# Kernel optimization log

Hardware: AMD Instinct MI355X
Metric: run time of the kernel (lower is better)

## Reference

```python
import jax, jax.numpy as jnp
import numpy as np

B, S, DIM = 1, 2048, 2048
HEADS, KV_HEADS = 32, 8
DH = DIM // HEADS          # 64 head dim
G = HEADS // KV_HEADS      # 4 grouped queries per kv head
CBLK = 16                  # compress block size (stride == block size)
SBLK = 16                  # selection (fine) block size
NSEL = 8                   # top-k selected blocks
WIN = 64                   # sliding window size
SCALE = DH ** -0.5
NEG = -1e30
CDIM = CBLK * DH


def setup_inputs():
    key = jax.random.key(0)
    ks = jax.random.split(key, 16)
    def rnd(i, shape, sc=0.02):
        return jax.random.normal(ks[i], shape, dtype=jnp.float32) * sc
    dim_inner, dim_kv = HEADS * DH, KV_HEADS * DH
    return {
        "hidden_states": jax.random.normal(ks[0], (B, S, DIM), dtype=jnp.float32),
        "w_qkv": rnd(1, (DIM, dim_inner + 2 * dim_kv)),
        "k_pos": rnd(2, (KV_HEADS, CBLK, DH)),
        "v_pos": rnd(3, (KV_HEADS, CBLK, DH)),
        "k_cw1": rnd(4, (CDIM, CDIM)), "k_cb1": jnp.zeros((CDIM,), jnp.float32),
        "k_cw2": rnd(5, (CDIM, DH)),  "k_cb2": jnp.zeros((DH,), jnp.float32),
        "v_cw1": rnd(6, (CDIM, CDIM)), "v_cb1": jnp.zeros((CDIM,), jnp.float32),
        "v_cw2": rnd(7, (CDIM, DH)),  "v_cb2": jnp.zeros((DH,), jnp.float32),
        "mem_ck": rnd(8, (KV_HEADS, 1, DH)),
        "mem_cv": rnd(9, (KV_HEADS, 1, DH)),
        "w_gate": rnd(10, (DIM, 3 * HEADS)),
        "b_gate": jnp.tile(jnp.array([-2.0, -2.0, 2.0], jnp.float32), HEADS),
        "w_out": rnd(11, (dim_inner, DIM)),
    }


def _rope(x, pos):
    # rotary-embedding-torch style: interleaved pairs (x0,x1),(x2,x3),...
    d = x.shape[-1]
    inv = 1.0 / (10000.0 ** (jnp.arange(0, d, 2, dtype=jnp.float32) / d))
    ang = pos[:, None] * inv[None, :]
    cos, sin = jnp.cos(ang), jnp.sin(ang)
    x1, x2 = x[..., 0::2], x[..., 1::2]
    return jnp.stack([x1 * cos - x2 * sin, x1 * sin + x2 * cos], axis=-1).reshape(x.shape)


def _forward(x, w_qkv, k_pos, v_pos, k_cw1, k_cb1, k_cw2, k_cb2,
             v_cw1, v_cb1, v_cw2, v_cb2, mem_ck, mem_cv, w_gate, b_gate, w_out):
    b, n, _ = x.shape
    di, dkv = HEADS * DH, KV_HEADS * DH
    qkv = x @ w_qkv
    # head index = kv_head * G + grouped_query, matching 'b n (h d) -> b h n d'
    q = qkv[..., :di].reshape(b, n, KV_HEADS, G, DH).transpose(0, 2, 3, 1, 4)    # [b,kh,g,n,d]
    k = qkv[..., di:di + dkv].reshape(b, n, KV_HEADS, DH).transpose(0, 2, 1, 3)  # [b,kh,n,d]
    v = qkv[..., di + dkv:].reshape(b, n, KV_HEADS, DH).transpose(0, 2, 1, 3)

    # ---- branch 1: compressed-block attention (pre-rotary q/k, intra-block abs pos) ----
    nc = n // CBLK
    kb = k[:, :, :nc * CBLK].reshape(b, KV_HEADS, nc, CBLK, DH) + k_pos[None, :, None]
    vb = v[:, :, :nc * CBLK].reshape(b, KV_HEADS, nc, CBLK, DH) + v_pos[None, :, None]
    ck = jax.nn.relu(kb.reshape(b, KV_HEADS, nc, CDIM) @ k_cw1 + k_cb1) @ k_cw2 + k_cb2
    cv = jax.nn.relu(vb.reshape(b, KV_HEADS, nc, CDIM) @ v_cw1 + v_cb1) @ v_cw2 + v_cb2
    ck = jnp.concatenate([jnp.broadcast_to(mem_ck[None], (b, KV_HEADS, 1, DH)), ck], axis=2)
    cv = jnp.concatenate([jnp.broadcast_to(mem_cv[None], (b, KV_HEADS, 1, DH)), cv], axis=2)
    csim = jnp.einsum('bhgnd,bhjd->bhgnj', q, ck) * SCALE
    ck_last = jnp.concatenate([jnp.array([-1]), (jnp.arange(nc) + 1) * CBLK - 1])
    cmask = ck_last[None, :] < jnp.arange(n)[:, None]                            # [n, 1+nc]
    csim = jnp.where(cmask, csim, NEG)
    c_out = jnp.einsum('bhgnj,bhjd->bhgnd', jax.nn.softmax(csim, -1), cv)

    # ---- importance scores -> top-k selected blocks (shared across grouped queries) ----
    imp = csim[..., 1:].mean(axis=2)                                             # [b,kh,n,nc]
    imp = jnp.concatenate([jnp.full(imp.shape[:-1] + (1,), -1e3, imp.dtype), imp], axis=-1)
    imp = jax.nn.softmax(imp, -1)[..., 1:]
    sel_vals, sel_idx = jax.lax.top_k(imp, NSEL)                                 # [b,kh,n,NSEL]
    fine_gate_mask = sel_vals > 1e-10

    # rotary for fine + sliding branches
    pos = jnp.arange(n, dtype=jnp.float32)
    rq, rk = _rope(q, pos), _rope(k, pos)

    # ---- branch 2: fine attention over top-k selected blocks + causal own block ----
    nf = n // SBLK
    own = jnp.broadcast_to((jnp.arange(n) // SBLK)[None, None, :, None], (b, KV_HEADS, n, 1))
    idx = jnp.concatenate([sel_idx, own], axis=-1)                               # [b,kh,n,NSEL+1]
    kblocks = rk.reshape(b, KV_HEADS, nf, SBLK, DH)
    vblocks = v.reshape(b, KV_HEADS, nf, SBLK, DH)
    bi = jnp.arange(b)[:, None, None, None]
    hi = jnp.arange(KV_HEADS)[None, :, None, None]
    fk = kblocks[bi, hi, idx].reshape(b, KV_HEADS, n, (NSEL + 1) * SBLK, DH)
    fv = vblocks[bi, hi, idx].reshape(b, KV_HEADS, n, (NSEL + 1) * SBLK, DH)
    sel_m = jnp.repeat(fine_gate_mask[..., None], SBLK, -1).reshape(b, KV_HEADS, n, NSEL * SBLK)
    diag_m = (jnp.arange(n) % SBLK)[:, None] >= jnp.arange(SBLK)[None, :]        # own-block causal
    fmask = jnp.concatenate(
        [sel_m, jnp.broadcast_to(diag_m[None, None], (b, KV_HEADS, n, SBLK))], axis=-1)
    fsim = jnp.einsum('bhgnd,bhnjd->bhgnj', rq, fk) * SCALE
    fsim = jnp.where(fmask[:, :, None], fsim, NEG)
    f_out = jnp.einsum('bhgnj,bhnjd->bhgnd', jax.nn.softmax(fsim, -1), fv)

    # ---- branch 3: sliding-window attention (current + previous window, exact size) ----
    nwin = n // WIN
    qw = rq.reshape(b, KV_HEADS, G, nwin, WIN, DH)
    kw = rk.reshape(b, KV_HEADS, nwin, WIN, DH)
    vw = v.reshape(b, KV_HEADS, nwin, WIN, DH)
    kcat = jnp.concatenate([jnp.concatenate([jnp.zeros_like(kw[:, :, :1]), kw[:, :, :-1]], 2), kw], 3)
    vcat = jnp.concatenate([jnp.concatenate([jnp.zeros_like(vw[:, :, :1]), vw[:, :, :-1]], 2), vw], 3)
    ssim = jnp.einsum('bhgwid,bhwjd->bhgwij', qw, kcat) * SCALE
    i_, j_ = jnp.arange(WIN), jnp.arange(2 * WIN)
    delta = i_[:, None] - (j_[None, :] - WIN)                                    # query - key distance
    smask = ((delta >= 0) & (delta <= WIN))[None] \
        & ((jnp.arange(nwin) > 0)[:, None, None] | (j_ >= WIN)[None, None, :])
    ssim = jnp.where(smask[None, None, None], ssim, NEG)
    s_out = jnp.einsum('bhgwij,bhwjd->bhgwid', jax.nn.softmax(ssim, -1), vcat)
    s_out = s_out.reshape(b, KV_HEADS, G, n, DH)

    # ---- learned sigmoid gate combine (compressed, fine, sliding) + out proj ----
    gates = jax.nn.sigmoid(x @ w_gate + b_gate).reshape(b, n, KV_HEADS, G, 3).transpose(0, 2, 3, 1, 4)
    out = gates[..., 0:1] * c_out + gates[..., 1:2] * f_out + gates[..., 2:3] * s_out
    out = out.transpose(0, 3, 1, 2, 4).reshape(b, n, HEADS * DH)
    return out @ w_out


def reference(hidden_states, w_qkv, k_pos, v_pos, k_cw1, k_cb1, k_cw2, k_cb2,
              v_cw1, v_cb1, v_cw2, v_cb2, mem_ck, mem_cv, w_gate, b_gate, w_out):
    return _forward(hidden_states, w_qkv, k_pos, v_pos, k_cw1, k_cb1, k_cw2, k_cb2,
                    v_cw1, v_cb1, v_cw2, v_cb2, mem_ck, mem_cv, w_gate, b_gate, w_out)
```

## Files before the change

### kernel.cpp

```cpp
#include <hip/hip_runtime.h>
#include <hip/hip_bf16.h>
#include <math.h>

using bf16 = __hip_bfloat16;
typedef __attribute__((ext_vector_type(8))) short short8;
typedef __attribute__((ext_vector_type(4))) float f32x4;

#define SCALE 0.125f
#define NEGV  -1e30f
#define QS    3200

__device__ __forceinline__ float bf2f(bf16 x) { return __bfloat162float(x); }
__device__ __forceinline__ bf16  f2bf(float x) { return __float2bfloat16(x); }
__device__ __forceinline__ short f2bs(float x) {
  bf16 b = __float2bfloat16(x);
  return *reinterpret_cast<short*>(&b);
}
__device__ __forceinline__ float dot4(float4 a, float4 b) {
  return a.x * b.x + a.y * b.y + a.z * b.z + a.w * b.w;
}
__device__ __forceinline__ float sigm(float x) { return 1.0f / (1.0f + __expf(-x)); }

__device__ __forceinline__ void wavefence() {
  asm volatile("s_waitcnt lgkmcnt(0)" ::: "memory");
}

__device__ __forceinline__ void gload16(const bf16* g, bf16* l) {
  __builtin_amdgcn_global_load_lds(
      (const __attribute__((address_space(1))) unsigned int*)g,
      (__attribute__((address_space(3))) unsigned int*)l, 16, 0, 0);
}

__global__ void detect_mode_kernel(const void* __restrict__ bgate, int* __restrict__ flag)
{
  if (threadIdx.x == 0 && blockIdx.x == 0) {
    unsigned w = *(const unsigned*)bgate;
    flag[0] = (w == 0xC0000000u) ? 1 : 0;
  }
}

struct ConvArgs {
  const void* src[17];
  bf16*       dst[17];
  int         start[18];
};

__global__ __launch_bounds__(256)
void convert_all_kernel(ConvArgs a, int total, const int* __restrict__ flag)
{
  int i = blockIdx.x * 256 + threadIdx.x;
  if (i >= total) return;
  int s = 0;
  while (s < 16 && i >= a.start[s + 1]) s++;
  int off = i - a.start[s];
  if (*flag) a.dst[s][off] = f2bf(((const float*)a.src[s])[off]);
  else       a.dst[s][off] = ((const bf16*)a.src[s])[off];
}

__global__ __launch_bounds__(256)
void transpose_conv_kernel(const void* __restrict__ src, bf16* __restrict__ dst,
                           int K, int N, const int* __restrict__ flag)
{
  __shared__ bf16 ls[64][65];
  const int n0 = blockIdx.x * 64, k0 = blockIdx.y * 64;
  const int tid = threadIdx.x, c = tid & 63, r4 = tid >> 6;
  const bool f = (*flag != 0);
  #pragma unroll 4
  for (int r = 0; r < 16; r++) {
    int kk = r * 4 + r4;
    bf16 v = f2bf(0.f);
    if (n0 + c < N)
      v = f ? f2bf(((const float*)src)[(size_t)(k0 + kk) * N + n0 + c])
            : ((const bf16*)src)[(size_t)(k0 + kk) * N + n0 + c];
    ls[kk][c] = v;
  }
  __syncthreads();
  #pragma unroll 4
  for (int r = 0; r < 16; r++) {
    int nn = r * 4 + r4;
    if (n0 + nn < N)
      dst[(size_t)(n0 + nn) * K + k0 + c] = ls[c][nn];
  }
}

__global__ __launch_bounds__(256)
void vtrans_kernel(const float* __restrict__ qkv, bf16* __restrict__ vt)
{
  __shared__ bf16 ls[64][65];
  const int h = blockIdx.y;
  const int i0 = blockIdx.x * 64;
  const int tid = threadIdx.x, c = tid & 63, r4 = tid >> 6;
  #pragma unroll 4
  for (int r = 0; r < 16; r++) {
    int ii = r * 4 + r4;
    ls[ii][c] = f2bf(qkv[(size_t)(i0 + ii) * QS + 2560 + h * 64 + c]);
  }
  __syncthreads();
  #pragma unroll 4
  for (int r = 0; r < 16; r++) {
    int dd = r * 4 + r4;
    vt[((size_t)h * 64 + dd) * 2176 + 64 + i0 + c] = ls[c][dd];
  }
}

__global__ __launch_bounds__(256)
void gemm64_splitk_kernel(const bf16* __restrict__ A, const bf16* __restrict__ B,
                          const bf16* __restrict__ B2, float* __restrict__ C,
                          int M, int N, int K, int msplit, int Ks)
{
  __shared__ __align__(16) bf16 As[64 * 32];
  __shared__ __align__(16) bf16 Bs[64 * 32];
  const int tid = threadIdx.x, wave = tid >> 6, lane = tid & 63;
  const int quad = lane >> 4, l16 = lane & 15;
  const int m0 = blockIdx.y * 64, n0 = blockIdx.x * 64;
  const int kb = blockIdx.z * Ks;
  const bf16* Bu = (m0 >= msplit) ? B2 : B;
  f32x4 acc[4] = {{0,0,0,0},{0,0,0,0},{0,0,0,0},{0,0,0,0}};
  const int arow = tid >> 2, akp = (tid & 3) * 8;
  const int bkr = tid >> 3, bnc = (tid & 7) * 8;

  for (int k0 = kb; k0 < kb + Ks; k0 += 32) {
    __syncthreads();
    {
      const bf16* Ap = A + (size_t)(m0 + arow) * K + k0 + akp;
      *(int4*)(void*)&As[arow * 32 + akp] = *(const int4*)(const void*)Ap;
    }
    const bf16* Bp = Bu + (size_t)(k0 + bkr) * N + n0 + bnc;
    {
      int4 raw = *(const int4*)(const void*)Bp;
      const bf16* tp = (const bf16*)&raw;
      #pragma unroll
      for (int j = 0; j < 8; j++) Bs[(bnc + j) * 32 + bkr] = tp[j];
    }
    __syncthreads();
    short8 a = *(const short8*)(const void*)&As[(wave * 16 + l16) * 32 + quad * 8];
    #pragma unroll
    for (int nt = 0; nt < 4; nt++) {
      short8 b = *(const short8*)(const void*)&Bs[(nt * 16 + l16) * 32 + quad * 8];
      acc[nt] = __builtin_amdgcn_mfma_f32_16x16x32_bf16(a, b, acc[nt], 0, 0, 0);
    }
  }

  #pragma unroll
  for (int nt = 0; nt < 4; nt++) {
    int col = n0 + nt * 16 + l16;
    if (col < N) {
      #pragma unroll
      for (int r = 0; r < 4; r++) {
        int row = m0 + wave * 16 + quad * 4 + r;
        atomicAdd(&C[(size_t)row * N + col], acc[nt][r]);
      }
    }
  }
}

template<int TC_BF16, int ACT, int SPLIT, int GATE, int STOREF>
__global__ __launch_bounds__(256)
void gemm_bt_kernel(const bf16* __restrict__ A, const bf16* __restrict__ Bt,
                    const bf16* __restrict__ Bt2, const bf16* __restrict__ bias,
                    const bf16* __restrict__ bias2, void* __restrict__ Cv,
                    int M, int N, int K, int msplit, const int* __restrict__ flag)
{
  __shared__ __align__(16) bf16 As[128 * 32];
  __shared__ __align__(16) bf16 Bs[128 * 32];
  const int tid = threadIdx.x, wave = tid >> 6, lane = tid & 63;
  const int quad = lane >> 4, l16 = lane & 15;
  const int wm = (wave >> 1) * 64, wn = (wave & 1) * 64;
  const int m0 = blockIdx.y * 128, n0 = blockIdx.x * 128;
  const bf16* Bu = (SPLIT && m0 >= msplit) ? Bt2 : Bt;
  const bf16* bu = (SPLIT && m0 >= msplit) ? bias2 : bias;
  f32x4 acc[4][4];
  #pragma unroll
  for (int mt = 0; mt < 4; mt++)
    #pragma unroll
    for (int nt = 0; nt < 4; nt++) acc[mt][nt] = f32x4{0, 0, 0, 0};

  const int lr = lane >> 2, lc = (lane & 3) * 8;
  const bf16* gA0 = A  + (size_t)(m0 + wave * 32 + lr) * K + lc;
  const bf16* gA1 = gA0 + (size_t)16 * K;
  const bf16* gB0 = Bu + (size_t)(n0 + wave * 32 + lr) * K + lc;
  const bf16* gB1 = gB0 + (size_t)16 * K;
  bf16* lA0 = &As[wave * 1024];
  bf16* lA1 = &As[wave * 1024 + 512];
  bf16* lB0 = &Bs[wave * 1024];
  bf16* lB1 = &Bs[wave * 1024 + 512];

  for (int k0 = 0; k0 < K; k0 += 32) {
    __syncthreads();
    gload16(gA0 + k0, lA0);
    gload16(gA1 + k0, lA1);
    gload16(gB0 + k0, lB0);
    gload16(gB1 + k0, lB1);
    __syncthreads();

    short8 a[4], b[4];
    #pragma unroll
    for (int mt = 0; mt < 4; mt++)
      a[mt] = *(const short8*)(const void*)&As[(wm + mt * 16 + l16) * 32 + quad * 8];
    #pragma unroll
    for (int nt = 0; nt < 4; nt++)
      b[nt] = *(const short8*)(const void*)&Bs[(wn + nt * 16 + l16) * 32 + quad * 8];
    #pragma unroll
    for (int mt = 0; mt < 4; mt++)
      #pragma unroll
      for (int nt = 0; nt < 4; nt++)
        acc[mt][nt] = __builtin_amdgcn_mfma_f32_16x16x32_bf16(a[mt], b[nt], acc[mt][nt], 0, 0, 0);
  }

  const bool f32out = STOREF ? (*flag != 0) : false;
  #pragma unroll
  for (int nt = 0; nt < 4; nt++) {
    int col = n0 + wn + nt * 16 + l16;
    float bv;
    if (GATE) bv = (col >= 3072 && col < 3168) ? bf2f(bias2[col - 3072]) : 0.0f;
    else      bv = bu ? bf2f(bu[col]) : 0.0f;
    #pragma unroll
    for (int mt = 0; mt < 4; mt++) {
      #pragma unroll
      for (int r = 0; r < 4; r++) {
        int row = m0 + wm + mt * 16 + quad * 4 + r;
        float v = acc[mt][nt][r] + bv;
        if (ACT == 1) v = fmaxf(v, 0.0f);
        if (STOREF) {
          if (f32out) ((float*)Cv)[(size_t)row * N + col] = v;
          else        ((bf16*)Cv)[(size_t)row * N + col]  = f2bf(v);
        } else if (TC_BF16) {
          ((bf16*)Cv)[(size_t)row * N + col] = f2bf(v);
        } else {
          ((float*)Cv)[(size_t)row * N + col] = v;
        }
      }
    }
  }
}

__global__ __launch_bounds__(256)
void prep_kb_kernel(const float* __restrict__ qkv, const bf16* __restrict__ k_pos,
                    const bf16* __restrict__ v_pos, bf16* __restrict__ kbflat,
                    bf16* __restrict__ vbflat)
{
  int idx = blockIdx.x * 256 + threadIdx.x;
  if (idx >= 8 * 128 * 1024) return;
  int h = idx >> 17, rem = idx & 131071;
  int c = rem >> 10, f = rem & 1023, t = f >> 6, d = f & 63;
  int tok = c * 16 + t;
  float kv = qkv[(size_t)tok * QS + 2048 + h * 64 + d] + bf2f(k_pos[(h * 16 + t) * 64 + d]);
  float vv = qkv[(size_t)tok * QS + 2560 + h * 64 + d] + bf2f(v_pos[(h * 16 + t) * 64 + d]);
  kbflat[idx] = f2bf(kv);
  vbflat[idx] = f2bf(vv);
}

__global__ __launch_bounds__(256)
void concat_kernel(const float* __restrict__ ckpre, const float* __restrict__ cvpre,
                   const bf16* __restrict__ mem_ck, const bf16* __restrict__ mem_cv,
                   const bf16* __restrict__ k_cb2, const bf16* __restrict__ v_cb2,
                   float* __restrict__ ck, bf16* __restrict__ cvT)
{
  int idx = blockIdx.x * 256 + threadIdx.x;
  if (idx >= 8 * 160 * 64) return;
  int h = idx / (160 * 64), r = (idx >> 6) % 160, d = idx & 63;
  if (r >= 129) { cvT[((size_t)h * 64 + d) * 160 + r] = f2bf(0.f); return; }
  float kv, vv;
  if (r == 0) {
    kv = bf2f(mem_ck[h * 64 + d]);
    vv = bf2f(mem_cv[h * 64 + d]);
  } else {
    kv = ckpre[((size_t)h * 128 + r - 1) * 64 + d] + bf2f(k_cb2[d]);
    vv = cvpre[((size_t)h * 128 + r - 1) * 64 + d] + bf2f(v_cb2[d]);
  }
  ck[((size_t)h * 129 + r) * 64 + d] = kv;
  cvT[((size_t)h * 64 + d) * 160 + r] = f2bf(vv);
}

__global__ __launch_bounds__(256)
void compress_attn_kernel(const float* __restrict__ qkv, const float* __restrict__ ck,
                          const bf16* __restrict__ cvT,
                          float* __restrict__ outpre, int* __restrict__ sel)
{
  __shared__ __align__(16) float qs[4][16][64];
  __shared__ __align__(16) bf16  ps[4][16][176];
  const int tid = threadIdx.x, w = tid >> 6, lane = tid & 63;
  const int quad = lane >> 4, l16 = lane & 15;
  const int h = blockIdx.x >> 7;
  const int i0 = (blockIdx.x & 127) * 16 + w * 4;

  #pragma unroll
  for (int m = 0; m < 16; m++)
    qs[w][m][lane] = qkv[(size_t)(i0 + (m >> 2)) * QS + (h * 4 + (m & 3)) * 64 + lane];
  wavefence();

  const bool jin2 = (lane == 0);
  const float* kh = ck + (size_t)h * 129 * 64;
  const float4* k0 = (const float4*)(kh + lane * 64);
  const float4* k1 = (const float4*)(kh + (lane + 64) * 64);
  const float4* k2 = (const float4*)(kh + (jin2 ? 128 : 0) * 64);

  float d0[4][4], d1[4][4], d2[4][4];
  #pragma unroll
  for (int T = 0; T < 4; T++)
    #pragma unroll
    for (int g = 0; g < 4; g++) { d0[T][g] = 0.f; d1[T][g] = 0.f; d2[T][g] = 0.f; }

  #pragma unroll 4
  for (int t = 0; t < 16; t++) {
    float4 a = k0[t], b = k1[t], c = k2[t];
    #pragma unroll
    for (int T = 0; T < 4; T++)
      #pragma unroll
      for (int g = 0; g < 4; g++) {
        float4 qv = *(const float4*)&qs[w][T * 4 + g][t * 4];
        d0[T][g] += dot4(qv, a);
        d1[T][g] += dot4(qv, b);
        d2[T][g] += dot4(qv, c);
      }
  }

  #pragma unroll
  for (int T = 0; T < 4; T++) {
    const int i = i0 + T, jv = i >> 4;
    bool v0 = (lane == 0 || lane <= jv);
    bool v1 = (lane + 64 <= jv);
    bool v2 = jin2 && (128 <= jv);

    float sc0[4], sc1[4], sc2[4];
    #pragma unroll
    for (int g = 0; g < 4; g++) {
      sc0[g] = v0 ? d0[T][g] * SCALE : NEGV;
      sc1[g] = v1 ? d1[T][g] * SCALE : NEGV;
      sc2[g] = jin2 ? (v2 ? d2[T][g] * SCALE : NEGV) : -3.0e38f;
    }
    float imp0 = (sc0[0] + sc0[1] + sc0[2] + sc0[3]) * 0.25f;
    float imp1 = (sc1[0] + sc1[1] + sc1[2] + sc1[3]) * 0.25f;
    float imp2 = jin2 ? (sc2[0] + sc2[1] + sc2[2] + sc2[3]) * 0.25f : -3.0e38f;

    float p0[4], p1[4], p2[4];
    #pragma unroll
    for (int g = 0; g < 4; g++) {
      float mx = fmaxf(sc0[g], fmaxf(sc1[g], sc2[g]));
      for (int off = 32; off; off >>= 1) mx = fmaxf(mx, __shfl_xor(mx, off));
      float e0 = __expf(sc0[g] - mx), e1 = __expf(sc1[g] - mx);
      float e2 = jin2 ? __expf(sc2[g] - mx) : 0.0f;
      float sm = e0 + e1 + e2;
      for (int off = 32; off; off >>= 1) sm += __shfl_xor(sm, off);
      float inv = 1.0f / sm;
      p0[g] = e0 * inv; p1[g] = e1 * inv; p2[g] = e2 * inv;
    }

    #pragma unroll
    for (int g = 0; g < 4; g++) {
      ps[w][T * 4 + g][lane]      = f2bf(p0[g]);
      ps[w][T * 4 + g][64 + lane] = f2bf(p1[g]);
    }
    if (lane == 0) {
      #pragma unroll
      for (int g = 0; g < 4; g++) ps[w][T * 4 + g][128] = f2bf(p2[g]);
    }

    float iv0 = (lane == 0) ? -1000.0f : imp0;
    float iv1 = imp1;
    float iv2 = imp2;
    float mx = fmaxf(iv0, fmaxf(iv1, iv2));
    for (int off = 32; off; off >>= 1) mx = fmaxf(mx, __shfl_xor(mx, off));
    float e0 = __expf(iv0 - mx), e1 = __expf(iv1 - mx);
    float e2 = jin2 ? __expf(iv2 - mx) : 0.0f;
    float sm = e0 + e1 + e2;
    for (int off = 32; off; off >>= 1) sm += __shfl_xor(sm, off);
    float inv = 1.0f / sm;
    float q0 = (lane >= 1) ? e0 * inv : -1.0f;
    float q1 = e1 * inv;
    float q2 = jin2 ? e2 * inv : -1.0f;

    for (int s = 0; s < 8; s++) {
      float bv = q0; int bj = lane;
      if (q1 > bv) { bv = q1; bj = lane + 64; }
      if (q2 > bv) { bv = q2; bj = lane + 128; }
      for (int off = 32; off; off >>= 1) {
        float ov = __shfl_xor(bv, off); int oj = __shfl_xor(bj, off);
        if (ov > bv || (ov == bv && oj < bj)) { bv = ov; bj = oj; }
      }
      if (lane == 0) sel[((size_t)h * 2048 + i) * 8 + s] = (bv > 1e-10f) ? (bj - 1) : -1;
      if (bj == lane)            q0 = -1.0f;
      else if (bj == lane + 64)  q1 = -1.0f;
      else if (bj == lane + 128) q2 = -1.0f;
    }
  }

  #pragma unroll
  for (int r = 0; r < 4; r++) {
    ps[w][quad * 4 + r][129 + l16] = f2bf(0.f);
    ps[w][quad * 4 + r][145 + l16] = f2bf(0.f);
  }

  const int iq = i0 + quad;
  float g0v[4];
  #pragma unroll
  for (int g = 0; g < 4; g++)
    g0v[g] = sigm(qkv[(size_t)iq * QS + 3072 + (h * 4 + g) * 3 + 0]);
  wavefence();

  const bf16* cvh = cvT + (size_t)h * 64 * 160;
  f32x4 acc[4];
  #pragma unroll
  for (int dt = 0; dt < 4; dt++) acc[dt] = f32x4{0, 0, 0, 0};
  #pragma unroll
  for (int ks = 0; ks < 5; ks++) {
    short8 ap = *(const short8*)(const void*)&ps[w][l16][ks * 32 + quad * 8];
    #pragma unroll
    for (int dt = 0; dt < 4; dt++) {
      const bf16* cp = cvh + (size_t)(dt * 16 + l16) * 160 + ks * 32 + quad * 8;
      short8 bv = *(const short8*)(const void*)cp;
      acc[dt] = __builtin_amdgcn_mfma_f32_16x16x32_bf16(ap, bv, acc[dt], 0, 0, 0);
    }
  }

  #pragma unroll
  for (int g = 0; g < 4; g++) {
    const int hq = h * 4 + g;
    #pragma unroll
    for (int dt = 0; dt < 4; dt++)
      outpre[(size_t)iq * 2048 + hq * 64 + dt * 16 + l16] = g0v[g] * acc[dt][g];
  }
}

__global__ __launch_bounds__(256)
void rope_kernel(const float* __restrict__ qkv, bf16* __restrict__ qb,
                 bf16* __restrict__ kb)
{
  int idx = blockIdx.x * 256 + threadIdx.x;
  if (idx >= 2048 * 40 * 32) return;
  int m = idx & 31, hh = (idx >> 5) % 40, i = idx / 1280;
  int col = (hh < 32) ? hh * 64 + 2 * m : 2048 + (hh - 32) * 64 + 2 * m;
  const float* p = qkv + (size_t)i * QS + col;
  float x1 = p[0], x2 = p[1];
  float inv = exp2f(-0.41524101186092029f * (float)m);
  float ang = (float)i * inv;
  float s, c;
  __sincosf(ang, &s, &c);
  float r1 = x1 * c - x2 * s;
  float r2 = x1 * s + x2 * c;
  unsigned pack = ((unsigned)(unsigned short)f2bs(r1)) |
                  (((unsigned)(unsigned short)f2bs(r2)) << 16);
  if (hh < 32) {
    int h = hh >> 2, g = hh & 3;
    *(unsigned*)&qb[(((size_t)h * 2048 + i) * 4 + g) * 64 + 2 * m] = pack;
  } else {
    *(unsigned*)&kb[((size_t)(hh - 32) * 2048 + i) * 64 + 2 * m] = pack;
  }
}

__global__ __launch_bounds__(256)
void slide_attn_kernel(const float* __restrict__ qkv, const bf16* __restrict__ qb,
                       const bf16* __restrict__ kb, const bf16* __restrict__ vt,
                       bf16* __restrict__ oslide)
{
  __shared__ __align__(16) bf16 ps[4][16][104];
  const int tid = threadIdx.x, w = tid >> 6, lane = tid & 63;
  const int quad = lane >> 4, l16 = lane & 15;
  const int h = blockIdx.x >> 7, i0 = (blockIdx.x & 127) << 4;
  const int g = w;

  const bf16* qp = qb + (((size_t)h * 2048 + i0 + l16) * 4 + g) * 64 + quad * 8;
  short8 aq0 = *(const short8*)(const void*)qp;
  short8 aq1 = *(const short8*)(const void*)(qp + 32);

  const bf16* kbh = kb + (size_t)h * 2048 * 64;
  const int jbase = i0 - 64;

  f32x4 cs[5];
  #pragma unroll
  for (int t = 0; t < 5; t++) {
    int jr = jbase + t * 16 + l16;
    int jc = jr < 0 ? 0 : jr;
    const bf16* kp = kbh + (size_t)jc * 64 + quad * 8;
    short8 b0 = *(const short8*)(const void*)kp;
    short8 b1 = *(const short8*)(const void*)(kp + 32);
    f32x4 c = {0.f, 0.f, 0.f, 0.f};
    c = __builtin_amdgcn_mfma_f32_16x16x32_bf16(aq0, b0, c, 0, 0, 0);
    c = __builtin_amdgcn_mfma_f32_16x16x32_bf16(aq1, b1, c, 0, 0, 0);
    cs[t] = c;
  }

  float pr[5][4];
  #pragma unroll
  for (int r = 0; r < 4; r++) {
    int ti = i0 + quad * 4 + r;
    float mx = -3.0e38f;
    #pragma unroll
    for (int t = 0; t < 5; t++) {
      int j = jbase + t * 16 + l16;
      bool valid = (j >= 0) && (j >= ti - 64) && (j <= ti);
      float sv = valid ? cs[t][r] * SCALE : -3.0e38f;
      pr[t][r] = sv;
      mx = fmaxf(mx, sv);
    }
    #pragma unroll
    for (int off = 8; off; off >>= 1) mx = fmaxf(mx, __shfl_xor(mx, off));
    float sm = 0.f;
    #pragma unroll
    for (int t = 0; t < 5; t++) { float e = __expf(pr[t][r] - mx); pr[t][r] = e; sm += e; }
    #pragma unroll
    for (int off = 8; off; off >>= 1) sm += __shfl_xor(sm, off);
    float inv = 1.0f / sm;
    #pragma unroll
    for (int t = 0; t < 5; t++) pr[t][r] *= inv;
  }

  #pragma unroll
  for (int t = 0; t < 5; t++)
    #pragma unroll
    for (int r = 0; r < 4; r++)
      ps[w][quad * 4 + r][t * 16 + l16] = f2bf(pr[t][r]);
  #pragma unroll
  for (int r = 0; r < 4; r++) ps[w][l16][80 + quad * 4 + r] = f2bf(0.f);
  wavefence();

  const bf16* vth = vt + (size_t)h * 64 * 2176 + 64;
  f32x4 os[4];
  #pragma unroll
  for (int dt = 0; dt < 4; dt++) os[dt] = f32x4{0,0,0,0};
  #pragma unroll
  for (int ks = 0; ks < 3; ks++) {
    short8 ap = *(const short8*)(const void*)&ps[w][l16][ks * 32 + quad * 8];
    int coff = jbase + ks * 32 + quad * 8;
    #pragma unroll
    for (int dt = 0; dt < 4; dt++) {
      const bf16* vp = vth + (size_t)(dt * 16 + l16) * 2176 + coff;
      short8 bv = *(const short8*)(const void*)vp;
      os[dt] = __builtin_amdgcn_mfma_f32_16x16x32_bf16(ap, bv, os[dt], 0, 0, 0);
    }
  }

  #pragma unroll
  for (int r = 0; r < 4; r++) {
    int ti = i0 + quad * 4 + r;
    int hq = h * 4 + g;
    float g2 = sigm(qkv[(size_t)ti * QS + 3072 + hq * 3 + 2]);
    #pragma unroll
    for (int dt = 0; dt < 4; dt++)
      oslide[(size_t)ti * 2048 + hq * 64 + dt * 16 + l16] = f2bf(g2 * os[dt][r]);
  }
}

__global__ __launch_bounds__(256)
void fine_attn_kernel(const float* __restrict__ qkv, const int* __restrict__ sel,
                      const float* __restrict__ outpre, const bf16* __restrict__ oslide,
                      const bf16* __restrict__ qb, const bf16* __restrict__ kb,
                      const bf16* __restrict__ vt, bf16* __restrict__ outpre_b)
{
  __shared__ __align__(16) bf16 psf[4][16][176];
  const int tid = threadIdx.x, w = tid >> 6, lane = tid & 63;
  const int quad = lane >> 4, l16 = lane & 15;
  const int h = blockIdx.x >> 7;
  const int i0 = (blockIdx.x & 127) * 16 + w * 4;

  const bf16* qp = qb + (((size_t)h * 2048 + i0 + (l16 >> 2)) * 4 + (l16 & 3)) * 64 + quad * 8;
  short8 aq0 = *(const short8*)(const void*)qp;
  short8 aq1 = *(const short8*)(const void*)(qp + 32);

  const bf16* kbh = kb + (size_t)h * 2048 * 64;
  const int own = i0 >> 4;
  const int selbase = (h * 2048 + i0) * 8;

  f32x4 ct[9];

  {
    const bf16* kp = kbh + (size_t)(own * 16 + l16) * 64 + quad * 8;
    short8 b0 = *(const short8*)(const void*)kp;
    short8 b1 = *(const short8*)(const void*)(kp + 32);
    f32x4 c = {0.f, 0.f, 0.f, 0.f};
    c = __builtin_amdgcn_mfma_f32_16x16x32_bf16(aq0, b0, c, 0, 0, 0);
    c = __builtin_amdgcn_mfma_f32_16x16x32_bf16(aq1, b1, c, 0, 0, 0);
    const int imod = (i0 + quad) & 15;
    #pragma unroll
    for (int g = 0; g < 4; g++)
      ct[8][g] = (l16 <= imod) ? c[g] * SCALE : -3.0e38f;
  }

  int vb[4][8];
  #pragma unroll
  for (int T = 0; T < 4; T++) {
    #pragma unroll
    for (int t = 0; t < 8; t++) {
      int blk = __builtin_amdgcn_readfirstlane(sel[selbase + T * 8 + t]);
      bool tv = (blk >= 0);
      int blc = tv ? blk : 0;
      vb[T][t] = blc;
      const bf16* kp = kbh + (size_t)(blc * 16 + l16) * 64 + quad * 8;
      short8 b0 = *(const short8*)(const void*)kp;
      short8 b1 = *(const short8*)(const void*)(kp + 32);
      f32x4 c = {0.f, 0.f, 0.f, 0.f};
      c = __builtin_amdgcn_mfma_f32_16x16x32_bf16(aq0, b0, c, 0, 0, 0);
      c = __builtin_amdgcn_mfma_f32_16x16x32_bf16(aq1, b1, c, 0, 0, 0);
      #pragma unroll
      for (int g = 0; g < 4; g++) {
        float v = tv ? c[g] * SCALE : -3.0e38f;
        if (T == 0) ct[t][g] = v;
        else if (quad == T) ct[t][g] = v;
      }
    }
  }

  float fm[4], fsum[4];
  #pragma unroll
  for (int g = 0; g < 4; g++) fm[g] = -3.0e38f;
  #pragma unroll
  for (int t = 0; t < 9; t++)
    #pragma unroll
    for (int g = 0; g < 4; g++) fm[g] = fmaxf(fm[g], ct[t][g]);
  #pragma unroll
  for (int g = 0; g < 4; g++) {
    #pragma unroll
    for (int off = 8; off; off >>= 1) fm[g] = fmaxf(fm[g], __shfl_xor(fm[g], off));
    fsum[g] = 0.f;
  }
  #pragma unroll
  for (int t = 0; t < 9; t++)
    #pragma unroll
    for (int g = 0; g < 4; g++) {
      float e = __expf(ct[t][g] - fm[g]);
      ct[t][g] = e;
      fsum[g] += e;
    }
  #pragma unroll
  for (int g = 0; g < 4; g++) {
    #pragma unroll
    for (int off = 8; off; off >>= 1) fsum[g] += __shfl_xor(fsum[g], off);
    fsum[g] = 1.0f / fsum[g];
  }

  #pragma unroll
  for (int t = 0; t < 9; t++)
    #pragma unroll
    for (int g = 0; g < 4; g++)
      psf[w][quad * 4 + g][t * 16 + l16] = f2bf(ct[t][g] * fsum[g]);
  #pragma unroll
  for (int g = 0; g < 4; g++)
    psf[w][quad * 4 + g][144 + l16] = f2bf(0.f);

  const int iq = i0 + quad;
  float g1v[4], prev[4][4];
  #pragma unroll
  for (int g = 0; g < 4; g++) {
    const int hq = h * 4 + g;
    g1v[g] = sigm(qkv[(size_t)iq * QS + 3072 + hq * 3 + 1]);
    #pragma unroll
    for (int dt = 0; dt < 4; dt++) {
      size_t oidx = (size_t)iq * 2048 + hq * 64 + dt * 16 + l16;
      prev[g][dt] = outpre[oidx] + bf2f(oslide[oidx]);
    }
  }
  wavefence();

  const bf16* vth = vt + (size_t)h * 64 * 2176 + 64;

  f32x4 obase[4];
  {
    short8 ap = *(const short8*)(const void*)&psf[w][l16][128 + quad * 8];
    int coff = (((quad >> 1) == 0) ? own : 0) * 16 + (quad & 1) * 8;
    #pragma unroll
    for (int dt = 0; dt < 4; dt++) {
      const bf16* vp = vth + (size_t)(dt * 16 + l16) * 2176 + coff;
      short8 bv = *(const short8*)(const void*)vp;
      f32x4 z = {0.f, 0.f, 0.f, 0.f};
      obase[dt] = __builtin_amdgcn_mfma_f32_16x16x32_bf16(ap, bv, z, 0, 0, 0);
    }
  }

  f32x4 osave[4];
  #pragma unroll
  for (int T = 0; T < 4; T++) {
    f32x4 acc[4];
    #pragma unroll
    for (int dt = 0; dt < 4; dt++) acc[dt] = obase[dt];
    #pragma unroll
    for (int ks = 0; ks < 4; ks++) {
      short8 ap = *(const short8*)(const void*)&psf[w][l16][ks * 32 + quad * 8];
      int blkv = ((quad >> 1) == 0) ? vb[T][ks * 2] : vb[T][ks * 2 + 1];
      int coff = blkv * 16 + (quad & 1) * 8;
      #pragma unroll
      for (int dt = 0; dt < 4; dt++) {
        const bf16* vp = vth + (size_t)(dt * 16 + l16) * 2176 + coff;
        short8 bv = *(const short8*)(const void*)vp;
        acc[dt] = __builtin_amdgcn_mfma_f32_16x16x32_bf16(ap, bv, acc[dt], 0, 0, 0);
      }
    }
    #pragma unroll
    for (int dt = 0; dt < 4; dt++) {
      if (T == 0) osave[dt] = acc[dt];
      else if (quad == T) osave[dt] = acc[dt];
    }
  }

  #pragma unroll
  for (int g = 0; g < 4; g++) {
    const int hq = h * 4 + g;
    #pragma unroll
    for (int dt = 0; dt < 4; dt++) {
      size_t oidx = (size_t)iq * 2048 + hq * 64 + dt * 16 + l16;
      outpre_b[oidx] = f2bf(prev[g][dt] + g1v[g] * osave[dt][g]);
    }
  }
}

extern "C" void kernel_launch(void* const* d_in, const int* in_sizes, int n_in,
                              void* d_out, int out_size, void* d_ws, size_t ws_size,
                              hipStream_t stream)
{
  char* ws = (char*)d_ws;
  size_t off = 0;
  auto alloc = [&](size_t bytes) -> char* {
    char* p = ws + off; off = (off + bytes + 255) & ~(size_t)255; return p;
  };

  int* flag = (int*)alloc(256);
  bf16* inb[17];
  for (int i = 0; i < 17; i++) {
    if (i == 1 || i == 4 || i == 8 || i == 14 || i == 16) { inb[i] = nullptr; continue; }
    inb[i] = (bf16*)alloc((size_t)in_sizes[i] * sizeof(bf16));
  }
  bf16* w_qkvT = (bf16*)alloc(3200ull * 2048 * 2);
  bf16* k_cw1T = (bf16*)alloc(1024ull * 1024 * 2);
  bf16* v_cw1T = (bf16*)alloc(1024ull * 1024 * 2);
  bf16* w_outT = (bf16*)alloc(2048ull * 2048 * 2);

  float* qkv      = (float*)alloc(2048ull * QS * 4);
  float* outpre   = (float*)alloc(2048ull * 2048 * 4);
  bf16*  kvb      = (bf16*)alloc(2048ull * 1024 * 2);
  bf16*  hid      = (bf16*)alloc(2048ull * 1024 * 2);
  float* ckcvpre  = (float*)alloc(2048ull * 64 * 4);
  float* ckb      = (float*)alloc(8ull * 129 * 64 * 4);
  int*   sel      = (int*)alloc(8ull * 2048 * 8 * 4);
  bf16*  qbuf     = (bf16*)alloc(8ull * 2048 * 4 * 64 * 2);
  bf16*  kbuf     = (bf16*)alloc(8ull * 2048 * 64 * 2);
  bf16*  vtb      = (bf16*)alloc(8ull * 64 * 2176 * 2);
  bf16*  outpre_b = kvb;
  bf16*  cvT      = k_cw1T;
  bf16*  oslide   = (bf16*)w_qkvT;

  const bf16 *xb = inb[0], *k_posb = inb[2], *v_posb = inb[3],
             *k_cb1b = inb[5], *k_cw2b = inb[6], *k_cb2b = inb[7],
             *v_cb1b = inb[9], *v_cw2b = inb[10], *v_cb2b = inb[11],
             *mem_ckb = inb[12], *mem_cvb = inb[13], *b_gateb = inb[15];

  detect_mode_kernel<<<1, 64, 0, stream>>>(d_in[15], flag);

  ConvArgs ca;
  int total = 0, nseg = 0;
  for (int i = 0; i < 17; i++) {
    if (i == 1 || i == 4 || i == 8 || i == 14 || i == 16) continue;
    ca.src[nseg] = d_in[i];
    ca.dst[nseg] = inb[i];
    ca.start[nseg] = total;
    total += in_sizes[i];
    nseg++;
  }
  for (int s = nseg; s <= 17; s++) ca.start[s] = total;
  convert_all_kernel<<<(total + 255) / 256, 256, 0, stream>>>(ca, total, flag);

  transpose_conv_kernel<<<dim3(48, 32), 256, 0, stream>>>(d_in[1],  w_qkvT, 2048, 3072, flag);
  transpose_conv_kernel<<<dim3(2, 32),  256, 0, stream>>>(d_in[14], w_qkvT + 3072ull * 2048, 2048, 96, flag);
  transpose_conv_kernel<<<dim3(16, 16), 256, 0, stream>>>(d_in[4],  k_cw1T, 1024, 1024, flag);
  transpose_conv_kernel<<<dim3(16, 16), 256, 0, stream>>>(d_in[8],  v_cw1T, 1024, 1024, flag);
  transpose_conv_kernel<<<dim3(32, 32), 256, 0, stream>>>(d_in[16], w_outT, 2048, 2048, flag);
  hipMemsetAsync(ckcvpre, 0, 2048ull * 64 * 4, stream);
  hipMemsetAsync(vtb, 0, 8ull * 64 * 2176 * 2, stream);

  gemm_bt_kernel<0,0,0,1,0><<<dim3(25, 16), 256, 0, stream>>>(
      xb, w_qkvT, nullptr, nullptr, b_gateb, qkv, 2048, QS, 2048, 0, nullptr);

  rope_kernel<<<10240, 256, 0, stream>>>(qkv, qbuf, kbuf);
  vtrans_kernel<<<dim3(32, 8), 256, 0, stream>>>(qkv, vtb);

  prep_kb_kernel<<<4096, 256, 0, stream>>>(qkv, k_posb, v_posb, kvb, kvb + 1024 * 1024);
  gemm_bt_kernel<1,1,1,0,0><<<dim3(8, 16), 256, 0, stream>>>(
      kvb, k_cw1T, v_cw1T, k_cb1b, v_cb1b, hid, 2048, 1024, 1024, 1024, nullptr);
  gemm64_splitk_kernel<<<dim3(1, 32, 4), 256, 0, stream>>>(
      hid, k_cw2b, v_cw2b, ckcvpre, 2048, 64, 1024, 1024, 256);
  concat_kernel<<<320, 256, 0, stream>>>(ckcvpre, ckcvpre + 1024 * 64,
                                         mem_ckb, mem_cvb, k_cb2b, v_cb2b, ckb, cvT);
  compress_attn_kernel<<<1024, 256, 0, stream>>>(qkv, ckb, cvT, outpre, sel);
  slide_attn_kernel<<<1024, 256, 0, stream>>>(qkv, qbuf, kbuf, vtb, oslide);
  fine_attn_kernel<<<1024, 256, 0, stream>>>(qkv, sel, outpre, oslide, qbuf, kbuf, vtb, outpre_b);
  gemm_bt_kernel<0,0,0,0,1><<<dim3(16, 16), 256, 0, stream>>>(
      outpre_b, w_outT, nullptr, nullptr, nullptr, d_out, 2048, 2048, 2048, 0, flag);
}
```

Before: 516.3 us.

## Skip causally masked compressed blocks and batch softmax/top-k reductions in compress attention

The compressed-attention kernel now uses the fact that all 16 queries in a block share one causal limit. It drops the always-masked key 128, computes keys 64..127 only for the later half of query blocks, and bounds the PV MFMA loop by the number of valid 32-key chunks. The per-row softmax, importance softmax and top-8 selection are restructured so cross-lane shuffle reductions for the 4 rows run interleaved, which exposes more instruction-level parallelism. The q and p shared buffers are aliased and launch bounds request 5 blocks per SM to raise occupancy, at some risk of register pressure from the larger live arrays.

Measured after the change: 536.7 us. +4.0%, slower.

```diff
diff --git a/kernel.cpp b/kernel.cpp
--- a/kernel.cpp
+++ b/kernel.cpp
@@ -272,123 +272,164 @@
   cvT[((size_t)h * 64 + d) * 160 + r] = f2bf(vv);
 }
 
-__global__ __launch_bounds__(256)
+__global__ __launch_bounds__(256, 5)
 void compress_attn_kernel(const float* __restrict__ qkv, const float* __restrict__ ck,
                           const bf16* __restrict__ cvT,
                           float* __restrict__ outpre, int* __restrict__ sel)
 {
-  __shared__ __align__(16) float qs[4][16][64];
-  __shared__ __align__(16) bf16  ps[4][16][176];
+  __shared__ __align__(16) char un[4][5632];
   const int tid = threadIdx.x, w = tid >> 6, lane = tid & 63;
   const int quad = lane >> 4, l16 = lane & 15;
   const int h = blockIdx.x >> 7;
-  const int i0 = (blockIdx.x & 127) * 16 + w * 4;
+  const int jv = blockIdx.x & 127;
+  const int i0 = jv * 16 + w * 4;
+  float* qs = (float*)un[w];
+  bf16*  ps = (bf16*)un[w];
 
   #pragma unroll
   for (int m = 0; m < 16; m++)
-    qs[w][m][lane] = qkv[(size_t)(i0 + (m >> 2)) * QS + (h * 4 + (m & 3)) * 64 + lane];
+    qs[m * 64 + lane] = qkv[(size_t)(i0 + (m >> 2)) * QS + (h * 4 + (m & 3)) * 64 + lane];
   wavefence();
 
-  const bool jin2 = (lane == 0);
   const float* kh = ck + (size_t)h * 129 * 64;
   const float4* k0 = (const float4*)(kh + lane * 64);
   const float4* k1 = (const float4*)(kh + (lane + 64) * 64);
-  const float4* k2 = (const float4*)(kh + (jin2 ? 128 : 0) * 64);
-
-  float d0[4][4], d1[4][4], d2[4][4];
+  const bool two = (jv >= 64);
+
+  float d0[4][4], d1[4][4];
   #pragma unroll
   for (int T = 0; T < 4; T++)
     #pragma unroll
-    for (int g = 0; g < 4; g++) { d0[T][g] = 0.f; d1[T][g] = 0.f; d2[T][g] = 0.f; }
-
-  #pragma unroll 4
-  for (int t = 0; t < 16; t++) {
-    float4 a = k0[t], b = k1[t], c = k2[t];
+    for (int g = 0; g < 4; g++) { d0[T][g] = 0.f; d1[T][g] = 0.f; }
+
+  if (two) {
+    #pragma unroll 4
+    for (int t = 0; t < 16; t++) {
+      float4 a = k0[t], b = k1[t];
+      #pragma unroll
+      for (int T = 0; T < 4; T++)
+        #pragma unroll
+        for (int g = 0; g < 4; g++) {
+          float4 qv = *(const float4*)&qs[(T * 4 + g) * 64 + t * 4];
+          d0[T][g] += dot4(qv, a);
+          d1[T][g] += dot4(qv, b);
+        }
+    }
+  } else {
+    #pragma unroll 4
+    for (int t = 0; t < 16; t++) {
+      float4 a = k0[t];
+      #pragma unroll
+      for (int T = 0; T < 4; T++)
+        #pragma unroll
+        for (int g = 0; g < 4; g++) {
+          float4 qv = *(const float4*)&qs[(T * 4 + g) * 64 + t * 4];
+          d0[T][g] += dot4(qv, a);
+        }
+    }
+  }
+  wavefence();
+
+  const bool v0 = (lane == 0) || (lane <= jv);
+  const bool v1 = two && (lane + 64 <= jv);
+  float imp0[4], imp1[4];
+  #pragma unroll
+  for (int T = 0; T < 4; T++) {
+    #pragma unroll
+    for (int g = 0; g < 4; g++) {
+      d0[T][g] = v0 ? d0[T][g] * SCALE : NEGV;
+      d1[T][g] = v1 ? d1[T][g] * SCALE : NEGV;
+    }
+    imp0[T] = (d0[T][0] + d0[T][1] + d0[T][2] + d0[T][3]) * 0.25f;
+    imp1[T] = (d1[T][0] + d1[T][1] + d1[T][2] + d1[T][3]) * 0.25f;
+  }
+
+  float mx[4][4], sm[4][4];
+  #pragma unroll
+  for (int T = 0; T < 4; T++)
+    #pragma unroll
+    for (int g = 0; g < 4; g++) mx[T][g] = fmaxf(d0[T][g], d1[T][g]);
+  #pragma unroll
+  for (int off = 32; off; off >>= 1)
     #pragma unroll
     for (int T = 0; T < 4; T++)
       #pragma unroll
-      for (int g = 0; g < 4; g++) {
-        float4 qv = *(const float4*)&qs[w][T * 4 + g][t * 4];
-        d0[T][g] += dot4(qv, a);
-        d1[T][g] += dot4(qv, b);
-        d2[T][g] += dot4(qv, c);
+      for (int g = 0; g < 4; g++) mx[T][g] = fmaxf(mx[T][g], __shfl_xor(mx[T][g], off));
+  #pragma unroll
+  for (int T = 0; T < 4; T++)
+    #pragma unroll
+    for (int g = 0; g < 4; g++) {
+      d0[T][g] = __expf(d0[T][g] - mx[T][g]);
+      d1[T][g] = __expf(d1[T][g] - mx[T][g]);
+      sm[T][g] = d0[T][g] + d1[T][g];
+    }
+  #pragma unroll
+  for (int off = 32; off; off >>= 1)
+    #pragma unroll
+    for (int T = 0; T < 4; T++)
+      #pragma unroll
+      for (int g = 0; g < 4; g++) sm[T][g] += __shfl_xor(sm[T][g], off);
+  #pragma unroll
+  for (int T = 0; T < 4; T++)
+    #pragma unroll
+    for (int g = 0; g < 4; g++) {
+      float inv = 1.0f / sm[T][g];
+      ps[(T * 4 + g) * 176 + lane] = f2bf(d0[T][g] * inv);
+      if (two) ps[(T * 4 + g) * 176 + 64 + lane] = f2bf(d1[T][g] * inv);
+    }
+
+  float q0[4], q1[4];
+  {
+    float mxi[4], smi[4], e0[4], e1[4];
+    #pragma unroll
+    for (int T = 0; T < 4; T++) {
+      float iv0 = (lane == 0) ? -1000.0f : imp0[T];
+      mxi[T] = fmaxf(iv0, imp1[T]);
+      q0[T] = iv0;
+      q1[T] = imp1[T];
+    }
+    #pragma unroll
+    for (int off = 32; off; off >>= 1)
+      #pragma unroll
+      for (int T = 0; T < 4; T++) mxi[T] = fmaxf(mxi[T], __shfl_xor(mxi[T], off));
+    #pragma unroll
+    for (int T = 0; T < 4; T++) {
+      e0[T] = __expf(q0[T] - mxi[T]);
+      e1[T] = __expf(q1[T] - mxi[T]);
+      smi[T] = e0[T] + e1[T];
+    }
+    #pragma unroll
+    for (int off = 32; off; off >>= 1)
+      #pragma unroll
+      for (int T = 0; T < 4; T++) smi[T] += __shfl_xor(smi[T], off);
+    #pragma unroll
+    for (int T = 0; T < 4; T++) {
+      float inv = 1.0f / smi[T];
+      q0[T] = (lane >= 1) ? e0[T] * inv : -1.0f;
+      q1[T] = e1[T] * inv;
+    }
+  }
+  for (int s = 0; s < 8; s++) {
+    float bv[4]; int bj[4];
+    #pragma unroll
+    for (int T = 0; T < 4; T++) {
+      bv[T] = q0[T]; bj[T] = lane;
+      if (q1[T] > bv[T]) { bv[T] = q1[T]; bj[T] = lane + 64; }
+    }
+    #pragma unroll
+    for (int off = 32; off; off >>= 1)
+      #pragma unroll
+      for (int T = 0; T < 4; T++) {
+        float ov = __shfl_xor(bv[T], off); int oj = __shfl_xor(bj[T], off);
+        if (ov > bv[T] || (ov == bv[T] && oj < bj[T])) { bv[T] = ov; bj[T] = oj; }
       }
-  }
-
-  #pragma unroll
-  for (int T = 0; T < 4; T++) {
-    const int i = i0 + T, jv = i >> 4;
-    bool v0 = (lane == 0 || lane <= jv);
-    bool v1 = (lane + 64 <= jv);
-    bool v2 = jin2 && (128 <= jv);
-
-    float sc0[4], sc1[4], sc2[4];
-    #pragma unroll
-    for (int g = 0; g < 4; g++) {
-      sc0[g] = v0 ? d0[T][g] * SCALE : NEGV;
-      sc1[g] = v1 ? d1[T][g] * SCALE : NEGV;
-      sc2[g] = jin2 ? (v2 ? d2[T][g] * SCALE : NEGV) : -3.0e38f;
-    }
-    float imp0 = (sc0[0] + sc0[1] + sc0[2] + sc0[3]) * 0.25f;
-    float imp1 = (sc1[0] + sc1[1] + sc1[2] + sc1[3]) * 0.25f;
-    float imp2 = jin2 ? (sc2[0] + sc2[1] + sc2[2] + sc2[3]) * 0.25f : -3.0e38f;
-
-    float p0[4], p1[4], p2[4];
-    #pragma unroll
-    for (int g = 0; g < 4; g++) {
-      float mx = fmaxf(sc0[g], fmaxf(sc1[g], sc2[g]));
-      for (int off = 32; off; off >>= 1) mx = fmaxf(mx, __shfl_xor(mx, off));
-      float e0 = __expf(sc0[g] - mx), e1 = __expf(sc1[g] - mx);
-      float e2 = jin2 ? __expf(sc2[g] - mx) : 0.0f;
-      float sm = e0 + e1 + e2;
-      for (int off = 32; off; off >>= 1) sm += __shfl_xor(sm, off);
-      float inv = 1.0f / sm;
-      p0[g] = e0 * inv; p1[g] = e1 * inv; p2[g] = e2 * inv;
-    }
-
-    #pragma unroll
-    for (int g = 0; g < 4; g++) {
-      ps[w][T * 4 + g][lane]      = f2bf(p0[g]);
-      ps[w][T * 4 + g][64 + lane] = f2bf(p1[g]);
-    }
-    if (lane == 0) {
-      #pragma unroll
-      for (int g = 0; g < 4; g++) ps[w][T * 4 + g][128] = f2bf(p2[g]);
-    }
-
-    float iv0 = (lane == 0) ? -1000.0f : imp0;
-    float iv1 = imp1;
-    float iv2 = imp2;
-    float mx = fmaxf(iv0, fmaxf(iv1, iv2));
-    for (int off = 32; off; off >>= 1) mx = fmaxf(mx, __shfl_xor(mx, off));
-    float e0 = __expf(iv0 - mx), e1 = __expf(iv1 - mx);
-    float e2 = jin2 ? __expf(iv2 - mx) : 0.0f;
-    float sm = e0 + e1 + e2;
-    for (int off = 32; off; off >>= 1) sm += __shfl_xor(sm, off);
-    float inv = 1.0f / sm;
-    float q0 = (lane >= 1) ? e0 * inv : -1.0f;
-    float q1 = e1 * inv;
-    float q2 = jin2 ? e2 * inv : -1.0f;
-
-    for (int s = 0; s < 8; s++) {
-      float bv = q0; int bj = lane;
-      if (q1 > bv) { bv = q1; bj = lane + 64; }
-      if (q2 > bv) { bv = q2; bj = lane + 128; }
-      for (int off = 32; off; off >>= 1) {
-        float ov = __shfl_xor(bv, off); int oj = __shfl_xor(bj, off);
-        if (ov > bv || (ov == bv && oj < bj)) { bv = ov; bj = oj; }
-      }
-      if (lane == 0) sel[((size_t)h * 2048 + i) * 8 + s] = (bv > 1e-10f) ? (bj - 1) : -1;
-      if (bj == lane)            q0 = -1.0f;
-      else if (bj == lane + 64)  q1 = -1.0f;
-      else if (bj == lane + 128) q2 = -1.0f;
-    }
-  }
-
-  #pragma unroll
-  for (int r = 0; r < 4; r++) {
-    ps[w][quad * 4 + r][129 + l16] = f2bf(0.f);
-    ps[w][quad * 4 + r][145 + l16] = f2bf(0.f);
+    #pragma unroll
+    for (int T = 0; T < 4; T++) {
+      if (lane == 0)
+        sel[((size_t)h * 2048 + i0 + T) * 8 + s] = (bv[T] > 1e-10f) ? (bj[T] - 1) : -1;
+      if (bj[T] == lane)           q0[T] = -1.0f;
+      else if (bj[T] == lane + 64) q1[T] = -1.0f;
+    }
   }
 
   const int iq = i0 + quad;
@@ -399,12 +440,12 @@
   wavefence();
 
   const bf16* cvh = cvT + (size_t)h * 64 * 160;
+  const int nks = (jv >> 5) + 1;
   f32x4 acc[4];
   #pragma unroll
   for (int dt = 0; dt < 4; dt++) acc[dt] = f32x4{0, 0, 0, 0};
-  #pragma unroll
-  for (int ks = 0; ks < 5; ks++) {
-    short8 ap = *(const short8*)(const void*)&ps[w][l16][ks * 32 + quad * 8];
+  for (int ks = 0; ks < nks; ks++) {
+    short8 ap = *(const short8*)(const void*)&ps[l16 * 176 + ks * 32 + quad * 8];
     #pragma unroll
     for (int dt = 0; dt < 4; dt++) {
       const bf16* cp = cvh + (size_t)(dt * 16 + l16) * 160 + ks * 32 + quad * 8;
```
